# Optimization experiments

Hardware: AMD Instinct MI355X
Metric: run time of the kernel (lower is better)

The kernel has to match this reference:

```python
import jax, jax.numpy as jnp
import numpy as np

B, NX, NC, D, H = 4, 1024, 154, 1536, 24
HD = D // H
MH = int(D * 4.0)
EPS = 1e-6


def setup_inputs() -> dict:
    key = jax.random.key(0)
    ks = jax.random.split(key, 20)
    s = lambda i, shape, fan: jax.random.normal(ks[i], shape, jnp.float32) * (1.0 / np.sqrt(fan))
    return {
        "x": jax.random.normal(ks[0], (B, NX, D), jnp.float32),
        "c": jax.random.normal(ks[1], (B, NC, D), jnp.float32),
        "vec": jax.random.normal(ks[2], (B, D), jnp.float32),
        "w_mod": s(3, (D, 6 * D), D), "b_mod": jnp.zeros((6 * D,), jnp.float32),
        "w_qkv_x": s(4, (D, 3 * D), D), "b_qkv_x": jnp.zeros((3 * D,), jnp.float32),
        "w_qkv_c": s(5, (D, 3 * D), D), "b_qkv_c": jnp.zeros((3 * D,), jnp.float32),
        "w_proj_x": s(6, (D, D), D), "b_proj_x": jnp.zeros((D,), jnp.float32),
        "w_proj_c": s(7, (D, D), D), "b_proj_c": jnp.zeros((D,), jnp.float32),
        "w1_x": s(8, (D, MH), D), "b1_x": jnp.zeros((MH,), jnp.float32),
        "w2_x": s(9, (MH, D), MH), "b2_x": jnp.zeros((D,), jnp.float32),
        "w1_c": s(10, (D, MH), D), "b1_c": jnp.zeros((MH,), jnp.float32),
        "w2_c": s(11, (MH, D), MH), "b2_c": jnp.zeros((D,), jnp.float32),
    }


def _ln(t):
    m = jnp.mean(t, axis=-1, keepdims=True)
    v = jnp.var(t, axis=-1, keepdims=True)
    return (t - m) * jax.lax.rsqrt(v + EPS)


def reference(x, c, vec, w_mod, b_mod, w_qkv_x, b_qkv_x, w_qkv_c, b_qkv_c,
              w_proj_x, b_proj_x, w_proj_c, b_proj_c,
              w1_x, b1_x, w2_x, b2_x, w1_c, b1_c, w2_c, b2_c):
    # adaLN modulation: silu(vec) @ W -> 6 chunks, each [B,1,D]
    mod = (jax.nn.silu(vec) @ w_mod + b_mod)[:, None, :]
    sh_x, sc_x, g_x, sh_c, sc_c, g_c = jnp.split(mod, 6, axis=2)

    x_n = _ln(x) * (1 + sc_x) + sh_x
    c_n = _ln(c) * (1 + sc_c) + sh_c

    def qkv(t, w, b, n):
        o = (t @ w + b).reshape(t.shape[0], n, 3, H, HD)
        return o[:, :, 0], o[:, :, 1], o[:, :, 2]  # each [B,N,H,HD]

    qx, kx, vx = qkv(x_n, w_qkv_x, b_qkv_x, NX)
    qc, kc, vc = qkv(c_n, w_qkv_c, b_qkv_c, NC)
    q = jnp.concatenate([qx, qc], axis=1)
    k = jnp.concatenate([kx, kc], axis=1)
    v = jnp.concatenate([vx, vc], axis=1)

    scale = HD ** -0.5
    attn = jnp.einsum("bshd,bthd->bhst", q, k) * scale
    attn = jax.nn.softmax(attn, axis=-1)
    o = jnp.einsum("bhst,bthd->bshd", attn, v).reshape(B, NX + NC, D)
    xo, co = o[:, :NX], o[:, NX:]

    x = x + g_x * (xo @ w_proj_x + b_proj_x)
    c = c + g_c * (co @ w_proj_c + b_proj_c)

    gelu = lambda t: jax.nn.gelu(t, approximate=True)
    x = x + (gelu(_ln(x) @ w1_x + b1_x) @ w2_x + b2_x)
    c = c + (gelu(_ln(c) @ w1_c + b1_c) @ w2_c + b2_c)
    return x, c
```

## Files before the change

### kernel.cpp

```cpp
#include <hip/hip_runtime.h>
#include <stdint.h>

typedef unsigned short u16;
typedef unsigned int u32;
typedef __attribute__((ext_vector_type(8))) short bf16x8;
typedef __attribute__((ext_vector_type(8))) unsigned short u16x8;
typedef __attribute__((ext_vector_type(2))) unsigned int u32x2;
typedef __attribute__((ext_vector_type(4))) float f32x4;

#define LB256 __launch_bounds__(256, 2)

#define BB 4
#define NX 1024
#define NC 154
#define NT 1178
#define NTP 1184
#define DD 1536
#define HH 24
#define MHD 6144
#define NQKV 4608
#define NMOD 9216
#define KSPL 6

__device__ __forceinline__ int imin(int a, int b) { return a < b ? a : b; }

__device__ __forceinline__ u16 f2bf(float f) {
  u32 u = __float_as_uint(f);
  u32 r = (u + 0x7fffu + ((u >> 16) & 1u)) >> 16;
  return (u16)r;
}

__device__ __forceinline__ float bf2f(u16 v) {
  u32 u = ((u32)v) << 16;
  return __uint_as_float(u);
}

__device__ __forceinline__ float gelu_t(float x) {
  float u = 1.5957691216f * x * fmaf(0.044715f, x * x, 1.f);
  return x / (1.f + __expf(-u));
}

__device__ __forceinline__ f32x4 fzero4() {
  f32x4 z; z[0] = 0.f; z[1] = 0.f; z[2] = 0.f; z[3] = 0.f; return z;
}

__device__ __forceinline__ void glds16(const u16* g, u16* l) {
  __builtin_amdgcn_global_load_lds(
      (const __attribute__((address_space(1))) void*)g,
      (__attribute__((address_space(3))) void*)l, 16, 0, 0);
}

#define WAITV4 asm volatile("s_waitcnt vmcnt(4)" ::: "memory")
#define WAITV0 asm volatile("s_waitcnt vmcnt(0)" ::: "memory")
#define SCHEDB __builtin_amdgcn_sched_barrier(0)

struct TDesc {
  const float* W[8];
  u16* Wt[8];
  int K[8];
  int N[8];
  int off[9];
};

__global__ void k_transpose8(TDesc d) {
  __shared__ float tile[32][33];
  int bid = blockIdx.x;
  int i = 0;
#pragma unroll
  for (int t = 1; t < 8; ++t)
    if (bid >= d.off[t]) i = t;
  const float* W = d.W[i];
  u16* Wt = d.Wt[i];
  const int K = d.K[i], N = d.N[i];
  const int local = bid - d.off[i];
  const int nbx = N >> 5;
  const int n0 = (local % nbx) * 32, k0 = (local / nbx) * 32;
  int tx = threadIdx.x & 31, ty = threadIdx.x >> 5;
#pragma unroll
  for (int j = 0; j < 32; j += 8)
    tile[ty + j][tx] = W[(size_t)(k0 + ty + j) * N + n0 + tx];
  __syncthreads();
#pragma unroll
  for (int j = 0; j < 32; j += 8)
    Wt[(size_t)(n0 + ty + j) * K + k0 + tx] = f2bf(tile[tx][ty + j]);
}

__global__ void k_mod_part(const float* __restrict__ vec, const float* __restrict__ w_mod,
                           float* __restrict__ part) {
  __shared__ float sv[BB][256];
  int n = blockIdx.x * 256 + threadIdx.x;
  int kb = blockIdx.y;
  int k0 = kb * 256;
  for (int i = threadIdx.x; i < BB * 256; i += 256) {
    int b = i >> 8, kk = i & 255;
    float v = vec[b * DD + k0 + kk];
    sv[b][kk] = v / (1.f + __expf(-v));
  }
  __syncthreads();
  float a0 = 0.f, a1 = 0.f, a2 = 0.f, a3 = 0.f;
  for (int k = 0; k < 256; ++k) {
    float w = w_mod[(size_t)(k0 + k) * NMOD + n];
    a0 = fmaf(sv[0][k], w, a0);
    a1 = fmaf(sv[1][k], w, a1);
    a2 = fmaf(sv[2][k], w, a2);
    a3 = fmaf(sv[3][k], w, a3);
  }
  part[((size_t)kb * BB + 0) * NMOD + n] = a0;
  part[((size_t)kb * BB + 1) * NMOD + n] = a1;
  part[((size_t)kb * BB + 2) * NMOD + n] = a2;
  part[((size_t)kb * BB + 3) * NMOD + n] = a3;
}

__global__ void k_mod_red(const float* __restrict__ part, const float* __restrict__ b_mod,
                          float* __restrict__ mod) {
  int n = blockIdx.x * 256 + threadIdx.x;
  float bb = b_mod[n];
#pragma unroll
  for (int b = 0; b < BB; ++b) {
    float s = bb;
#pragma unroll
    for (int kb = 0; kb < KSPL; ++kb) s += part[((size_t)kb * BB + b) * NMOD + n];
    mod[b * NMOD + n] = s;
  }
}

__global__ LB256 void k_ln(const float* __restrict__ in, u16* __restrict__ out,
                           const float* __restrict__ modp, int sh_off, int sc_off,
                           int rows_per_b) {
  int row = blockIdx.x;
  int b = row / rows_per_b;
  const float* xr = in + (size_t)row * DD;
  float v[6];
  float s = 0.f, s2 = 0.f;
#pragma unroll
  for (int i = 0; i < 6; ++i) {
    float t = xr[threadIdx.x + 256 * i];
    v[i] = t; s += t; s2 += t * t;
  }
#pragma unroll
  for (int m = 32; m >= 1; m >>= 1) {
    s += __shfl_xor(s, m);
    s2 += __shfl_xor(s2, m);
  }
  __shared__ float red[8];
  int wid = threadIdx.x >> 6;
  if ((threadIdx.x & 63) == 0) { red[wid] = s; red[4 + wid] = s2; }
  __syncthreads();
  s = red[0] + red[1] + red[2] + red[3];
  s2 = red[4] + red[5] + red[6] + red[7];
  float mean = s * (1.f / (float)DD);
  float var = s2 * (1.f / (float)DD) - mean * mean;
  float rstd = rsqrtf(var + 1e-6f);
#pragma unroll
  for (int i = 0; i < 6; ++i) {
    int d = threadIdx.x + 256 * i;
    float y = (v[i] - mean) * rstd;
    if (modp) y = y * (1.f + modp[b * NMOD + sc_off + d]) + modp[b * NMOD + sh_off + d];
    out[(size_t)row * DD + d] = f2bf(y);
  }
}

template <int EPI>
__device__ __forceinline__ void gemm_epi(
    const f32x4 (&acc)[4][4], int m0, int n0, int wm, int wn, int g, int r,
    int M, int N, const float* bias, void* outp, const float* resid,
    const float* modp, int goff, int rpb, int zed,
    u16* qb, u16* kb, u16* vtb) {
#pragma unroll
  for (int mi = 0; mi < 4; ++mi) {
#pragma unroll
    for (int ni = 0; ni < 4; ++ni) {
      const int col = n0 + wn + ni * 16 + r;
      float bv = 0.f;
      if constexpr (EPI != 4) bv = bias[col];
#pragma unroll
      for (int j = 0; j < 4; ++j) {
        const int row = m0 + wm + mi * 16 + g * 4 + j;
        if (row >= M) continue;
        const size_t off = (size_t)row * N + col;
        float v = acc[mi][ni][j] + bv;
        if constexpr (EPI == 0) {
          ((u16*)outp)[off] = f2bf(v);
        } else if constexpr (EPI == 1) {
          ((u16*)outp)[off] = f2bf(gelu_t(v));
        } else if constexpr (EPI == 2) {
          const int b = row / rpb;
          ((float*)outp)[off] = resid[off] + modp[b * NMOD + goff + col] * v;
        } else if constexpr (EPI == 3) {
          ((float*)outp)[off] = resid[off] + v;
        } else if constexpr (EPI == 4) {
          ((u16*)outp)[(size_t)zed * (size_t)goff + off] = f2bf(acc[mi][ni][j]);
        } else {
          const int b = row / rpb;
          const int t = goff + (row - b * rpb);
          const u16 bw = f2bf(v);
          if (col < DD) {
            const int h = col >> 6, d = col & 63;
            qb[(((size_t)b * HH + h) * NT + t) * 64 + d] = bw;
          } else if (col < 2 * DD) {
            const int cc = col - DD;
            const int h = cc >> 6, d = cc & 63;
            kb[(((size_t)b * HH + h) * NT + t) * 64 + d] = bw;
          } else {
            const int cc = col - 2 * DD;
            const int h = cc >> 6, d = cc & 63;
            vtb[((size_t)b * HH + h) * (64 * NTP) + (size_t)d * NTP + t] = bw;
          }
        }
      }
    }
  }
}

template <int EPI1, int EPI2>
__global__ LB256 void k_gemm2(
    const u16* __restrict__ A1, const u16* __restrict__ Bt1, const float* __restrict__ bias1,
    int M1, int rpb1, int goff1, int kLen1,
    const u16* __restrict__ A2, const u16* __restrict__ Bt2, const float* __restrict__ bias2,
    int M2, int rpb2, int goff2, int kLen2,
    int yHi, int N, int lda, int ldb, int kzOff,
    void* __restrict__ out1, void* __restrict__ out2,
    const float* __restrict__ resid1, const float* __restrict__ resid2,
    const float* __restrict__ modp,
    u16* __restrict__ qb, u16* __restrict__ kb, u16* __restrict__ vtb) {
  __shared__ __align__(16) u16 sm[3 * 8192];
  const int tid = threadIdx.x;
  const int lane = tid & 63;
  const int g = lane >> 4, r = lane & 15;
  const int wid = tid >> 6;

  const int gx = gridDim.x;
  const int nwg = gx * gridDim.y;
  int wg = blockIdx.y * gx + blockIdx.x;
  {
    int q = nwg >> 3, rr = nwg & 7;
    int xcd = wg & 7, sl = wg >> 3;
    wg = (xcd < rr ? xcd * (q + 1) : rr * (q + 1) + (xcd - rr) * q) + sl;
  }
  const int mIdx = wg / gx;
  const bool role2 = mIdx >= yHi;

  const u16* A = role2 ? A2 : A1;
  const u16* Bt = role2 ? Bt2 : Bt1;
  const int M = role2 ? M2 : M1;
  const int kLen = role2 ? kLen2 : kLen1;
  const int m0 = (role2 ? (mIdx - yHi) : mIdx) * 128, n0 = (wg % gx) * 128;
  const int wm = (wid >> 1) * 64, wn = (wid & 1) * 64;
  A += (size_t)blockIdx.z * kzOff;
  Bt += (size_t)blockIdx.z * kzOff;

  f32x4 acc[4][4];
#pragma unroll
  for (int i = 0; i < 4; ++i)
#pragma unroll
    for (int j = 0; j < 4; ++j) acc[i][j] = fzero4();

  const int rl = lane >> 2;
  const int slg = (lane & 3) ^ ((lane >> 3) & 3);
  const int c0 = wid * 2, c1 = wid * 2 + 1;
  const size_t aR0 = (size_t)imin(m0 + c0 * 16 + rl, M - 1) * lda + slg * 8;
  const size_t aR1 = (size_t)imin(m0 + c1 * 16 + rl, M - 1) * lda + slg * 8;
  const size_t bR0 = (size_t)(n0 + c0 * 16 + rl) * ldb + slg * 8;
  const size_t bR1 = (size_t)(n0 + c1 * 16 + rl) * ldb + slg * 8;

  int aOff[4], bOff[4];
#pragma unroll
  for (int mi = 0; mi < 4; ++mi) aOff[mi] = (wm + mi * 16 + r) * 32 + ((g ^ ((r >> 1) & 3)) * 8);
#pragma unroll
  for (int ni = 0; ni < 4; ++ni) bOff[ni] = 4096 + (wn + ni * 16 + r) * 32 + ((g ^ ((r >> 1) & 3)) * 8);

  const int nt = kLen >> 5;

#define STAGE(BI, T)                                        \
  do {                                                      \
    u16* bb = &sm[(BI) * 8192];                             \
    size_t kk = (size_t)(T) * 32;                           \
    glds16(A + aR0 + kk, bb + c0 * 512);                    \
    glds16(A + aR1 + kk, bb + c1 * 512);                    \
    glds16(Bt + bR0 + kk, bb + 4096 + c0 * 512);            \
    glds16(Bt + bR1 + kk, bb + 4096 + c1 * 512);            \
  } while (0)

  STAGE(0, 0);
  STAGE(1, 1);

  for (int t = 0; t < nt - 1; ++t) {
    WAITV4;
    __builtin_amdgcn_s_barrier();
    SCHEDB;
    if (t + 2 < nt) STAGE((t + 2) % 3, t + 2);
    const u16* bb = &sm[(t % 3) * 8192];
    bf16x8 af[4], bfr[4];
#pragma unroll
    for (int mi = 0; mi < 4; ++mi) af[mi] = *(const bf16x8*)(bb + aOff[mi]);
#pragma unroll
    for (int ni = 0; ni < 4; ++ni) bfr[ni] = *(const bf16x8*)(bb + bOff[ni]);
    __builtin_amdgcn_s_setprio(1);
#pragma unroll
    for (int mi = 0; mi < 4; ++mi)
#pragma unroll
      for (int ni = 0; ni < 4; ++ni)
        acc[mi][ni] = __builtin_amdgcn_mfma_f32_16x16x32_bf16(af[mi], bfr[ni], acc[mi][ni], 0, 0, 0);
    __builtin_amdgcn_s_setprio(0);
    SCHEDB;
  }
  {
    WAITV0;
    __builtin_amdgcn_s_barrier();
    SCHEDB;
    const u16* bb = &sm[((nt - 1) % 3) * 8192];
    bf16x8 af[4], bfr[4];
#pragma unroll
    for (int mi = 0; mi < 4; ++mi) af[mi] = *(const bf16x8*)(bb + aOff[mi]);
#pragma unroll
    for (int ni = 0; ni < 4; ++ni) bfr[ni] = *(const bf16x8*)(bb + bOff[ni]);
#pragma unroll
    for (int mi = 0; mi < 4; ++mi)
#pragma unroll
      for (int ni = 0; ni < 4; ++ni)
        acc[mi][ni] = __builtin_amdgcn_mfma_f32_16x16x32_bf16(af[mi], bfr[ni], acc[mi][ni], 0, 0, 0);
  }
#undef STAGE

  if (role2)
    gemm_epi<EPI2>(acc, m0, n0, wm, wn, g, r, M, N, bias2, out2, resid2, modp,
                   goff2, rpb2, blockIdx.z, qb, kb, vtb);
  else
    gemm_epi<EPI1>(acc, m0, n0, wm, wn, g, r, M, N, bias1, out1, resid1, modp,
                   goff1, rpb1, blockIdx.z, qb, kb, vtb);
}

__global__ void k_red2(const u16* __restrict__ p0x, const u16* __restrict__ p1x,
                       const float* __restrict__ residx, const float* __restrict__ bx,
                       const u16* __restrict__ p0c, const u16* __restrict__ p1c,
                       const float* __restrict__ residc, const float* __restrict__ bc,
                       float* __restrict__ outx, float* __restrict__ outc) {
  int row = blockIdx.x;
  if (row < BB * NX) {
    size_t base = (size_t)row * DD;
#pragma unroll
    for (int i = 0; i < 6; ++i) {
      int j = threadIdx.x + 256 * i;
      outx[base + j] = residx[base + j] + bx[j] + bf2f(p0x[base + j]) + bf2f(p1x[base + j]);
    }
  } else {
    size_t base = (size_t)(row - BB * NX) * DD;
#pragma unroll
    for (int i = 0; i < 6; ++i) {
      int j = threadIdx.x + 256 * i;
      outc[base + j] = residc[base + j] + bc[j] + bf2f(p0c[base + j]) + bf2f(p1c[base + j]);
    }
  }
}

__global__ __launch_bounds__(512, 2) void k_attn(
    const u16* __restrict__ q, const u16* __restrict__ kk,
    const u16* __restrict__ vt, u16* __restrict__ ox, u16* __restrict__ oc) {
  __shared__ __align__(16) u16 Ks[64][72];
  __shared__ __align__(16) u16 Vs[64][72];
  __shared__ __align__(16) u16 Ps[8][16][72];

  const int lane = threadIdx.x & 63, wid = threadIdx.x >> 6;
  const int g = lane >> 4, r = lane & 15;
  const int q0 = blockIdx.x * 128;
  const int h = blockIdx.y, b = blockIdx.z;
  const size_t bh = (size_t)b * HH + h;
  const u16* qp = q + bh * (NT * 64);
  const u16* kp = kk + bh * (NT * 64);
  const u16* vp = vt + bh * (64 * NTP);

  const int qrow = imin(q0 + wid * 16 + r, NT - 1);
  u16x8 qr0 = *(const u16x8*)(qp + (size_t)qrow * 64 + g * 8);
  u16x8 qr1 = *(const u16x8*)(qp + (size_t)qrow * 64 + 32 + g * 8);
  bf16x8 qa0, qa1;
#pragma unroll
  for (int e = 0; e < 8; ++e) {
    qa0[e] = (short)f2bf(bf2f(qr0[e]) * 0.125f);
    qa1[e] = (short)f2bf(bf2f(qr1[e]) * 0.125f);
  }

  f32x4 oacc[4];
#pragma unroll
  for (int i = 0; i < 4; ++i) oacc[i] = fzero4();
  float mrow = -1e30f, lrow = 0.f;

  const int trA = threadIdx.x >> 3;
  const int ccA = (threadIdx.x & 7) * 8;

  u16x8 kreg, vreg;
#define LOADKV(T0)                                                     \
  do {                                                                 \
    int tsrc = imin((T0) + trA, NT - 1);                               \
    kreg = *(const u16x8*)(kp + (size_t)tsrc * 64 + ccA);              \
    int tcol = (T0) + ccA;                                             \
    if (tcol + 8 <= NT) {                                              \
      vreg = *(const u16x8*)(vp + (size_t)trA * NTP + tcol);           \
    } else {                                                           \
      _Pragma("unroll")                                                \
      for (int e = 0; e < 8; ++e)                                      \
        vreg[e] = vp[(size_t)trA * NTP + imin(tcol + e, NT - 1)];      \
    }                                                                  \
  } while (0)

  LOADKV(0);

  for (int t0 = 0; t0 < NT; t0 += 64) {
    if (t0) __syncthreads();
    *(u16x8*)&Ks[trA][ccA] = kreg;
    *(u16x8*)&Vs[trA][ccA] = vreg;
    __syncthreads();
    if (t0 + 64 < NT) LOADKV(t0 + 64);

    f32x4 s[4];
#pragma unroll
    for (int ni = 0; ni < 4; ++ni) {
      s[ni] = fzero4();
      s[ni] = __builtin_amdgcn_mfma_f32_16x16x32_bf16(*(const bf16x8*)&Ks[ni * 16 + r][g * 8], qa0, s[ni], 0, 0, 0);
      s[ni] = __builtin_amdgcn_mfma_f32_16x16x32_bf16(*(const bf16x8*)&Ks[ni * 16 + r][32 + g * 8], qa1, s[ni], 0, 0, 0);
    }

    float pv[4][4];
    float pm = -1e30f;
#pragma unroll
    for (int ni = 0; ni < 4; ++ni)
#pragma unroll
      for (int j = 0; j < 4; ++j) {
        int t = t0 + ni * 16 + g * 4 + j;
        float sv = (t < NT) ? s[ni][j] : -1e30f;
        pv[ni][j] = sv;
        pm = fmaxf(pm, sv);
      }
    pm = fmaxf(pm, __shfl_xor(pm, 16));
    pm = fmaxf(pm, __shfl_xor(pm, 32));

    float mn = fmaxf(mrow, pm);
    float alpha = __expf(mrow - mn);
    mrow = mn;
    float rs = 0.f;
#pragma unroll
    for (int ni = 0; ni < 4; ++ni)
#pragma unroll
      for (int j = 0; j < 4; ++j) {
        float p = __expf(pv[ni][j] - mn);
        pv[ni][j] = p;
        rs += p;
      }
    rs += __shfl_xor(rs, 16);
    rs += __shfl_xor(rs, 32);
    lrow = lrow * alpha + rs;

#pragma unroll
    for (int j = 0; j < 4; ++j) {
      float aj = __shfl(alpha, g * 4 + j);
#pragma unroll
      for (int ni = 0; ni < 4; ++ni) oacc[ni][j] *= aj;
    }

#pragma unroll
    for (int ni = 0; ni < 4; ++ni) {
      u32x2 w;
      w[0] = (u32)f2bf(pv[ni][0]) | ((u32)f2bf(pv[ni][1]) << 16);
      w[1] = (u32)f2bf(pv[ni][2]) | ((u32)f2bf(pv[ni][3]) << 16);
      *(u32x2*)&Ps[wid][r][ni * 16 + g * 4] = w;
    }

    bf16x8 pa0 = *(const bf16x8*)&Ps[wid][r][g * 8];
    bf16x8 pa1 = *(const bf16x8*)&Ps[wid][r][32 + g * 8];
#pragma unroll
    for (int ni = 0; ni < 4; ++ni) {
      oacc[ni] = __builtin_amdgcn_mfma_f32_16x16x32_bf16(pa0, *(const bf16x8*)&Vs[ni * 16 + r][g * 8], oacc[ni], 0, 0, 0);
      oacc[ni] = __builtin_amdgcn_mfma_f32_16x16x32_bf16(pa1, *(const bf16x8*)&Vs[ni * 16 + r][32 + g * 8], oacc[ni], 0, 0, 0);
    }
  }
#undef LOADKV

  float linv[4];
#pragma unroll
  for (int j = 0; j < 4; ++j) linv[j] = 1.f / __shfl(lrow, g * 4 + j);

#pragma unroll
  for (int ni = 0; ni < 4; ++ni)
#pragma unroll
    for (int j = 0; j < 4; ++j) {
      int tq = q0 + wid * 16 + g * 4 + j;
      if (tq >= NT) continue;
      float val = oacc[ni][j] * linv[j];
      int col = h * 64 + ni * 16 + r;
      if (tq < NX)
        ox[(size_t)(b * NX + tq) * DD + col] = f2bf(val);
      else
        oc[(size_t)(b * NC + tq - NX) * DD + col] = f2bf(val);
    }
}

extern "C" void kernel_launch(void* const* d_in, const int* in_sizes, int n_in,
                              void* d_out, int out_size, void* d_ws, size_t ws_size,
                              hipStream_t stream) {
  const float* x = (const float*)d_in[0];
  const float* c = (const float*)d_in[1];
  const float* vec = (const float*)d_in[2];
  const float* w_mod = (const float*)d_in[3];
  const float* b_mod = (const float*)d_in[4];
  const float* w_qkv_x = (const float*)d_in[5];
  const float* b_qkv_x = (const float*)d_in[6];
  const float* w_qkv_c = (const float*)d_in[7];
  const float* b_qkv_c = (const float*)d_in[8];
  const float* w_proj_x = (const float*)d_in[9];
  const float* b_proj_x = (const float*)d_in[10];
  const float* w_proj_c = (const float*)d_in[11];
  const float* b_proj_c = (const float*)d_in[12];
  const float* w1_x = (const float*)d_in[13];
  const float* b1_x = (const float*)d_in[14];
  const float* w2_x = (const float*)d_in[15];
  const float* b2_x = (const float*)d_in[16];
  const float* w1_c = (const float*)d_in[17];
  const float* b1_c = (const float*)d_in[18];
  const float* w2_c = (const float*)d_in[19];
  const float* b2_c = (const float*)d_in[20];

  if (ws_size < 229195776ull) return;

  char* ws = (char*)d_ws;
  u16* wt_qkv_x = (u16*)(ws + 0);
  u16* wt_qkv_c = (u16*)(ws + 14155776);
  u16* wt_proj_x = (u16*)(ws + 28311552);
  u16* wt_proj_c = (u16*)(ws + 33030144);
  u16* wt_w1_x = (u16*)(ws + 37748736);
  u16* wt_w1_c = (u16*)(ws + 56623104);
  u16* wt_w2_x = (u16*)(ws + 75497472);
  u16* wt_w2_c = (u16*)(ws + 94371840);
  float* modf = (float*)(ws + 113246208);
  char* S = ws + 113393664;
  u16* xn = (u16*)(S);
  u16* cn = (u16*)(S + 12582912);
  float* x2 = (float*)(S + 14475264);
  float* c2 = (float*)(S + 39641088);
  u16* pb0 = (u16*)(S);
  u16* pc0 = (u16*)(S + 12582912);
  u16* pb1 = (u16*)(S + 43425792);
  u16* pc1 = (u16*)(S + 56008704);
  const int PSTRIDE = 43425792 / 2;
  u16* qb = (u16*)(S + 57901056);
  u16* kb = (u16*)(S + 72376320);
  u16* vtb = (u16*)(S + 86851584);
  u16* hx = (u16*)(S + 57901056);
  u16* hc = (u16*)(S + 108232704);
  float* modpart = (float*)(S + 57901056);

  {
    TDesc d;
    const float* Ws[8] = {w_qkv_x, w_qkv_c, w_proj_x, w_proj_c, w1_x, w1_c, w2_x, w2_c};
    u16* Wts[8] = {wt_qkv_x, wt_qkv_c, wt_proj_x, wt_proj_c, wt_w1_x, wt_w1_c, wt_w2_x, wt_w2_c};
    int Ks[8] = {DD, DD, DD, DD, DD, DD, MHD, MHD};
    int Ns[8] = {NQKV, NQKV, DD, DD, MHD, MHD, DD, DD};
    int off = 0;
    for (int i = 0; i < 8; ++i) {
      d.W[i] = Ws[i]; d.Wt[i] = Wts[i]; d.K[i] = Ks[i]; d.N[i] = Ns[i];
      d.off[i] = off;
      off += (Ns[i] >> 5) * (Ks[i] >> 5);
    }
    d.off[8] = off;
    k_transpose8<<<dim3(off), 256, 0, stream>>>(d);
  }

  k_mod_part<<<dim3(NMOD / 256, KSPL), 256, 0, stream>>>(vec, w_mod, modpart);
  k_mod_red<<<dim3(NMOD / 256), 256, 0, stream>>>(modpart, b_mod, modf);

  k_ln<<<dim3(BB * NX), 256, 0, stream>>>(x, xn, modf, 0, DD, NX);
  k_ln<<<dim3(BB * NC), 256, 0, stream>>>(c, cn, modf, 3 * DD, 4 * DD, NC);

  k_gemm2<5, 5><<<dim3(NQKV / 128, 37), 256, 0, stream>>>(
      xn, wt_qkv_x, b_qkv_x, BB * NX, NX, 0, DD,
      cn, wt_qkv_c, b_qkv_c, BB * NC, NC, NX, DD,
      32, NQKV, DD, DD, 0, nullptr, nullptr, nullptr, nullptr, nullptr,
      qb, kb, vtb);

  k_attn<<<dim3((NT + 127) / 128, HH, BB), 512, 0, stream>>>(qb, kb, vtb, xn, cn);

  k_gemm2<2, 2><<<dim3(DD / 128, 37), 256, 0, stream>>>(
      xn, wt_proj_x, b_proj_x, BB * NX, NX, 2 * DD, DD,
      cn, wt_proj_c, b_proj_c, BB * NC, NC, 5 * DD, DD,
      32, DD, DD, DD, 0, x2, c2, x, c, modf, nullptr, nullptr, nullptr);

  k_ln<<<dim3(BB * NX), 256, 0, stream>>>(x2, xn, nullptr, 0, 0, NX);
  k_ln<<<dim3(BB * NC), 256, 0, stream>>>(c2, cn, nullptr, 0, 0, NC);

  k_gemm2<1, 1><<<dim3(MHD / 128, 37), 256, 0, stream>>>(
      xn, wt_w1_x, b1_x, BB * NX, NX, 0, DD,
      cn, wt_w1_c, b1_c, BB * NC, NC, 0, DD,
      32, MHD, DD, DD, 0, hx, hc, nullptr, nullptr, nullptr, nullptr, nullptr, nullptr);

  float* outx = (float*)d_out;
  float* outc = outx + (size_t)BB * NX * DD;
  k_gemm2<4, 4><<<dim3(DD / 128, 37, 2), 256, 0, stream>>>(
      hx, wt_w2_x, b2_x, BB * NX, NX, PSTRIDE, MHD / 2,
      hc, wt_w2_c, b2_c, BB * NC, NC, PSTRIDE, MHD / 2,
      32, DD, MHD, MHD, MHD / 2, pb0, pc0, nullptr, nullptr, nullptr,
      nullptr, nullptr, nullptr);
  k_red2<<<dim3(BB * (NX + NC)), 256, 0, stream>>>(
      pb0, pb1, x2, b2_x, pc0, pc1, c2, b2_c, outx, outc);
}
```

Before: 689.0 us.

## Vectorize transpose and LayerNorm accesses, group GEMM tiles into column panels

The weight transpose kernel and the LayerNorm kernel now move data with float2 loads and packed 32-bit bf16 stores, cutting the number of memory instructions. The GEMM work-group mapping now walks tiles in panels eight N-tiles wide, going down M inside each panel. This keeps B columns and A rows resident in L2 while they are reused. The transpose change adds 2-way LDS bank conflicts on the strided tile reads, and the panel mapping adds integer division work per block.

```diff
diff --git a/kernel.cpp b/kernel.cpp
--- a/kernel.cpp
+++ b/kernel.cpp
@@ -75,14 +75,20 @@
   const int local = bid - d.off[i];
   const int nbx = N >> 5;
   const int n0 = (local % nbx) * 32, k0 = (local / nbx) * 32;
-  int tx = threadIdx.x & 31, ty = threadIdx.x >> 5;
-#pragma unroll
-  for (int j = 0; j < 32; j += 8)
-    tile[ty + j][tx] = W[(size_t)(k0 + ty + j) * N + n0 + tx];
+  const int cx = threadIdx.x & 15, ry = threadIdx.x >> 4;
+#pragma unroll
+  for (int j = 0; j < 32; j += 16) {
+    float2 t2 = *(const float2*)&W[(size_t)(k0 + ry + j) * N + n0 + cx * 2];
+    tile[ry + j][cx * 2] = t2.x;
+    tile[ry + j][cx * 2 + 1] = t2.y;
+  }
   __syncthreads();
 #pragma unroll
-  for (int j = 0; j < 32; j += 8)
-    Wt[(size_t)(n0 + ty + j) * K + k0 + tx] = f2bf(tile[tx][ty + j]);
+  for (int j = 0; j < 32; j += 16) {
+    const int ny = ry + j;
+    u32 w = (u32)f2bf(tile[cx * 2][ny]) | ((u32)f2bf(tile[cx * 2 + 1][ny]) << 16);
+    *(u32*)&Wt[(size_t)(n0 + ny) * K + k0 + cx * 2] = w;
+  }
 }
 
 __global__ void k_mod_part(const float* __restrict__ vec, const float* __restrict__ w_mod,
@@ -129,13 +135,15 @@
                            int rows_per_b) {
   int row = blockIdx.x;
   int b = row / rows_per_b;
-  const float* xr = in + (size_t)row * DD;
-  float v[6];
+  const float2* xr = (const float2*)(in + (size_t)row * DD);
+  float2 v[3];
   float s = 0.f, s2 = 0.f;
 #pragma unroll
-  for (int i = 0; i < 6; ++i) {
-    float t = xr[threadIdx.x + 256 * i];
-    v[i] = t; s += t; s2 += t * t;
+  for (int i = 0; i < 3; ++i) {
+    float2 t = xr[threadIdx.x + 256 * i];
+    v[i] = t;
+    s += t.x + t.y;
+    s2 += t.x * t.x + t.y * t.y;
   }
 #pragma unroll
   for (int m = 32; m >= 1; m >>= 1) {
@@ -152,11 +160,18 @@
   float var = s2 * (1.f / (float)DD) - mean * mean;
   float rstd = rsqrtf(var + 1e-6f);
 #pragma unroll
-  for (int i = 0; i < 6; ++i) {
-    int d = threadIdx.x + 256 * i;
-    float y = (v[i] - mean) * rstd;
-    if (modp) y = y * (1.f + modp[b * NMOD + sc_off + d]) + modp[b * NMOD + sh_off + d];
-    out[(size_t)row * DD + d] = f2bf(y);
+  for (int i = 0; i < 3; ++i) {
+    int d = (threadIdx.x + 256 * i) * 2;
+    float y0 = (v[i].x - mean) * rstd;
+    float y1 = (v[i].y - mean) * rstd;
+    if (modp) {
+      float2 sc = *(const float2*)&modp[b * NMOD + sc_off + d];
+      float2 sh = *(const float2*)&modp[b * NMOD + sh_off + d];
+      y0 = y0 * (1.f + sc.x) + sh.x;
+      y1 = y1 * (1.f + sc.y) + sh.y;
+    }
+    u32 w = (u32)f2bf(y0) | ((u32)f2bf(y1) << 16);
+    *(u32*)&out[(size_t)row * DD + d] = w;
   }
 }
 
@@ -230,21 +245,36 @@
   const int wid = tid >> 6;
 
   const int gx = gridDim.x;
-  const int nwg = gx * gridDim.y;
+  const int gyTot = gridDim.y;
+  const int nwg = gx * gyTot;
   int wg = blockIdx.y * gx + blockIdx.x;
   {
     int q = nwg >> 3, rr = nwg & 7;
     int xcd = wg & 7, sl = wg >> 3;
     wg = (xcd < rr ? xcd * (q + 1) : rr * (q + 1) + (xcd - rr) * q) + sl;
   }
-  const int mIdx = wg / gx;
+  int mIdx, nIdx;
+  {
+    const int np1 = (gx - 1) >> 3;
+    const int lastw = gx - np1 * 8;
+    const int full = gyTot * 8;
+    if (wg < np1 * full) {
+      int p = wg / full, off = wg % full;
+      mIdx = off >> 3;
+      nIdx = p * 8 + (off & 7);
+    } else {
+      int off = wg - np1 * full;
+      mIdx = off / lastw;
+      nIdx = np1 * 8 + off % lastw;
+    }
+  }
   const bool role2 = mIdx >= yHi;
 
   const u16* A = role2 ? A2 : A1;
   const u16* Bt = role2 ? Bt2 : Bt1;
   const int M = role2 ? M2 : M1;
   const int kLen = role2 ? kLen2 : kLen1;
-  const int m0 = (role2 ? (mIdx - yHi) : mIdx) * 128, n0 = (wg % gx) * 128;
+  const int m0 = (role2 ? (mIdx - yHi) : mIdx) * 128, n0 = nIdx * 128;
   const int wm = (wid >> 1) * 64, wn = (wid & 1) * 64;
   A += (size_t)blockIdx.z * kzOff;
   Bt += (size_t)blockIdx.z * kzOff;
```

Result: faster. 674.6 us (-2.1%).
